# Kernel optimization log

Hardware: AMD Instinct MI355X
Metric: run time of the kernel (lower is better)

Reference implementation:

```python
import jax, jax.numpy as jnp
import numpy as np

N = 16777216  # 2^24 samples


def setup_inputs() -> dict:
    key = jax.random.key(0)
    k1, k2 = jax.random.split(key)
    confidences = jax.random.uniform(k1, (N,), dtype=jnp.float32)
    accuracies = jax.random.randint(k2, (N,), 0, 2).astype(jnp.float32)
    return {"confidences": confidences, "accuracies": accuracies, "num_bins": 15}


def reference(confidences, accuracies, num_bins):
    # Bin b covers (b/num_bins, (b+1)/num_bins]; ceil(c*num_bins)-1 gives that bin.
    # Values outside (0, 1] fall in no bin (matches the torch strict/inclusive bounds)
    # and are routed to an overflow segment that is dropped.
    n = confidences.shape[0]
    idx = jnp.ceil(confidences * num_bins).astype(jnp.int32) - 1
    valid = (confidences > 0.0) & (confidences <= 1.0)
    idx = jnp.where(valid, jnp.clip(idx, 0, num_bins - 1), num_bins)
    sum_conf = jax.ops.segment_sum(confidences, idx, num_segments=num_bins + 1)[:num_bins]
    sum_acc = jax.ops.segment_sum(accuracies, idx, num_segments=num_bins + 1)[:num_bins]
    # ece = sum_b |avg_conf_b - avg_acc_b| * (cnt_b / n) = sum_b |sum_conf_b - sum_acc_b| / n
    # Empty bins have zero sums and contribute 0, matching the prop_in_bin > 0 guard.
    ece = jnp.sum(jnp.abs(sum_conf - sum_acc)) / n
    return ece
```

## Files before the change

kernel.cpp:

```cpp
#include <hip/hip_runtime.h>


#define NB 15

__global__ __launch_bounds__(256) void ece_hist(
        const float* __restrict__ conf,
        const float* __restrict__ acc,
        float* __restrict__ partials,
        int n4, int n, int nblocks) {
    float bins[NB];
#pragma unroll
    for (int b = 0; b < NB; ++b) bins[b] = 0.0f;

    const float4* __restrict__ c4 = (const float4*)conf;
    const float4* __restrict__ a4 = (const float4*)acc;
    const int stride = gridDim.x * blockDim.x;

    for (int i = blockIdx.x * blockDim.x + threadIdx.x; i < n4; i += stride) {
        float4 c = c4[i];
        float4 a = a4[i];
        float cv[4] = {c.x, c.y, c.z, c.w};
        float av[4] = {a.x, a.y, a.z, a.w};
#pragma unroll
        for (int j = 0; j < 4; ++j) {
            float v = cv[j];
            float d = v - av[j];
            int idx = (int)ceilf(v * 15.0f) - 1;
            bool valid = (v > 0.0f) && (v <= 1.0f);
            idx = valid ? idx : -1;
#pragma unroll
            for (int b = 0; b < NB; ++b)
                bins[b] += (idx == b) ? d : 0.0f;
        }
    }

    if (blockIdx.x == 0) {
        for (int i = n4 * 4 + (int)threadIdx.x; i < n; i += blockDim.x) {
            float v = conf[i];
            float d = v - acc[i];
            int idx = (int)ceilf(v * 15.0f) - 1;
            bool valid = (v > 0.0f) && (v <= 1.0f);
            idx = valid ? idx : -1;
#pragma unroll
            for (int b = 0; b < NB; ++b)
                bins[b] += (idx == b) ? d : 0.0f;
        }
    }

#pragma unroll
    for (int b = 0; b < NB; ++b) {
        float v = bins[b];
#pragma unroll
        for (int off = 32; off > 0; off >>= 1)
            v += __shfl_down(v, off, 64);
        bins[b] = v;
    }

    __shared__ float wsum[4][NB];
    const int wave = threadIdx.x >> 6;
    const int lane = threadIdx.x & 63;
    if (lane == 0) {
#pragma unroll
        for (int b = 0; b < NB; ++b) wsum[wave][b] = bins[b];
    }
    __syncthreads();

    if (threadIdx.x < NB) {
        float s = wsum[0][threadIdx.x] + wsum[1][threadIdx.x]
                + wsum[2][threadIdx.x] + wsum[3][threadIdx.x];
        partials[threadIdx.x * nblocks + blockIdx.x] = s;
    }
}

__global__ __launch_bounds__(960) void ece_final(
        const float* __restrict__ partials,
        float* __restrict__ out, int nblocks, float inv_n) {
    __shared__ float bsum[NB];
    const int wave = threadIdx.x >> 6;
    const int lane = threadIdx.x & 63;

    float s = 0.0f;
    for (int i = lane; i < nblocks; i += 64)
        s += partials[wave * nblocks + i];
#pragma unroll
    for (int off = 32; off > 0; off >>= 1)
        s += __shfl_down(s, off, 64);
    if (lane == 0) bsum[wave] = s;
    __syncthreads();

    if (threadIdx.x == 0) {
        float t = 0.0f;
#pragma unroll
        for (int b = 0; b < NB; ++b) t += fabsf(bsum[b]);
        out[0] = t * inv_n;
    }
}

extern "C" void kernel_launch(void* const* d_in, const int* in_sizes, int n_in,
                              void* d_out, int out_size, void* d_ws, size_t ws_size,
                              hipStream_t stream) {
    const float* conf = (const float*)d_in[0];
    const float* acc  = (const float*)d_in[1];
    float* partials   = (float*)d_ws;
    float* out        = (float*)d_out;

    const int n  = in_sizes[0];
    const int n4 = n / 4;

    int nblocks = 2048;
    while ((size_t)NB * nblocks * sizeof(float) > ws_size && nblocks > 1)
        nblocks >>= 1;
    int max_grid = (n4 + 255) / 256;
    if (nblocks > max_grid) nblocks = max_grid;
    if (nblocks < 1) nblocks = 1;

    ece_hist<<<nblocks, 256, 0, stream>>>(conf, acc, partials, n4, n, nblocks);
    ece_final<<<1, 960, 0, stream>>>(partials, out, nblocks, 1.0f / (float)n);
}
```

Before: 159.5 us.

## Replace per-thread select-based bins with per-wave LDS atomic histograms

Each element used to be added into all 15 register bins through a compare-and-select chain, which is heavy on VALU work. Now each element does one relaxed workgroup-scope float atomic add into a per-wave shared-memory histogram, with a 16th dump bin for out-of-range values. This also removes the wave shuffle reductions at the end. The main loop is unrolled to issue four float4 loads per array per iteration, giving more memory-level parallelism. The cost is contention: many lanes hit the same few LDS addresses, so the atomics serialise, and float summation order becomes nondeterministic.

```diff
diff --git a/kernel.cpp b/kernel.cpp
--- a/kernel.cpp
+++ b/kernel.cpp
@@ -2,72 +2,68 @@
 
 
 #define NB 15
+
+__device__ __forceinline__ void proc4(float4 c, float4 a, float* __restrict__ h) {
+    float cv[4] = {c.x, c.y, c.z, c.w};
+    float av[4] = {a.x, a.y, a.z, a.w};
+#pragma unroll
+    for (int j = 0; j < 4; ++j) {
+        float v = cv[j];
+        float d = v - av[j];
+        int t = (int)ceilf(v * 15.0f) - 1;
+        int idx = ((unsigned)t > 14u) ? 15 : t;
+        __hip_atomic_fetch_add(&h[idx], d, __ATOMIC_RELAXED,
+                               __HIP_MEMORY_SCOPE_WORKGROUP);
+    }
+}
 
 __global__ __launch_bounds__(256) void ece_hist(
         const float* __restrict__ conf,
         const float* __restrict__ acc,
         float* __restrict__ partials,
         int n4, int n, int nblocks) {
-    float bins[NB];
-#pragma unroll
-    for (int b = 0; b < NB; ++b) bins[b] = 0.0f;
+    __shared__ float hist[4][16];
+    if (threadIdx.x < 64) ((float*)hist)[threadIdx.x] = 0.0f;
+    __syncthreads();
+
+    float* h = hist[threadIdx.x >> 6];
 
     const float4* __restrict__ c4 = (const float4*)conf;
     const float4* __restrict__ a4 = (const float4*)acc;
     const int stride = gridDim.x * blockDim.x;
+    int i = blockIdx.x * blockDim.x + threadIdx.x;
 
-    for (int i = blockIdx.x * blockDim.x + threadIdx.x; i < n4; i += stride) {
-        float4 c = c4[i];
-        float4 a = a4[i];
-        float cv[4] = {c.x, c.y, c.z, c.w};
-        float av[4] = {a.x, a.y, a.z, a.w};
-#pragma unroll
-        for (int j = 0; j < 4; ++j) {
-            float v = cv[j];
-            float d = v - av[j];
-            int idx = (int)ceilf(v * 15.0f) - 1;
-            bool valid = (v > 0.0f) && (v <= 1.0f);
-            idx = valid ? idx : -1;
-#pragma unroll
-            for (int b = 0; b < NB; ++b)
-                bins[b] += (idx == b) ? d : 0.0f;
+    for (; i + 3 * stride < n4; i += 4 * stride) {
+        float4 c0 = c4[i];
+        float4 c1 = c4[i + stride];
+        float4 c2 = c4[i + 2 * stride];
+        float4 c3 = c4[i + 3 * stride];
+        float4 a0 = a4[i];
+        float4 a1 = a4[i + stride];
+        float4 a2 = a4[i + 2 * stride];
+        float4 a3 = a4[i + 3 * stride];
+        proc4(c0, a0, h);
+        proc4(c1, a1, h);
+        proc4(c2, a2, h);
+        proc4(c3, a3, h);
+    }
+    for (; i < n4; i += stride) proc4(c4[i], a4[i], h);
+
+    if (blockIdx.x == 0) {
+        for (int k = n4 * 4 + (int)threadIdx.x; k < n; k += blockDim.x) {
+            float v = conf[k];
+            float d = v - acc[k];
+            int t = (int)ceilf(v * 15.0f) - 1;
+            int idx = ((unsigned)t > 14u) ? 15 : t;
+            __hip_atomic_fetch_add(&h[idx], d, __ATOMIC_RELAXED,
+                                   __HIP_MEMORY_SCOPE_WORKGROUP);
         }
     }
 
-    if (blockIdx.x == 0) {
-        for (int i = n4 * 4 + (int)threadIdx.x; i < n; i += blockDim.x) {
-            float v = conf[i];
-            float d = v - acc[i];
-            int idx = (int)ceilf(v * 15.0f) - 1;
-            bool valid = (v > 0.0f) && (v <= 1.0f);
-            idx = valid ? idx : -1;
-#pragma unroll
-            for (int b = 0; b < NB; ++b)
-                bins[b] += (idx == b) ? d : 0.0f;
-        }
-    }
-
-#pragma unroll
-    for (int b = 0; b < NB; ++b) {
-        float v = bins[b];
-#pragma unroll
-        for (int off = 32; off > 0; off >>= 1)
-            v += __shfl_down(v, off, 64);
-        bins[b] = v;
-    }
-
-    __shared__ float wsum[4][NB];
-    const int wave = threadIdx.x >> 6;
-    const int lane = threadIdx.x & 63;
-    if (lane == 0) {
-#pragma unroll
-        for (int b = 0; b < NB; ++b) wsum[wave][b] = bins[b];
-    }
     __syncthreads();
-
     if (threadIdx.x < NB) {
-        float s = wsum[0][threadIdx.x] + wsum[1][threadIdx.x]
-                + wsum[2][threadIdx.x] + wsum[3][threadIdx.x];
+        float s = hist[0][threadIdx.x] + hist[1][threadIdx.x]
+                + hist[2][threadIdx.x] + hist[3][threadIdx.x];
         partials[threadIdx.x * nblocks + blockIdx.x] = s;
     }
 }
```

New measurement: 204.4 us. +28.2%, slower.
